# Kernel tuning notes

Measured on AMD Instinct MI355X. Metric: run time of the kernel, lower is better.

The kernel has to match this reference:

```python
import jax, jax.numpy as jnp
import numpy as np

B, T, DIM = 2, 2048, 2048
N_HEADS, N_KV_HEADS = 16, 4
HEAD_DIM = DIM // N_HEADS  # 128
N_REP = N_HEADS // N_KV_HEADS  # 4
ROPE_THETA = 10000.0


def setup_inputs() -> dict:
    key = jax.random.key(0)
    ks = jax.random.split(key, 5)
    x = jax.random.normal(ks[0], (B, T, DIM), dtype=jnp.float32)
    # RoPE tables (equivalent to complex freqs_cis = exp(i * t * inv_freq))
    inv_freq = 1.0 / (ROPE_THETA ** (np.arange(0, HEAD_DIM, 2, dtype=np.float32) / HEAD_DIM))
    t = np.arange(T, dtype=np.float32)
    ang = np.outer(t, inv_freq)  # (T, HEAD_DIM//2)
    freqs_cos = jnp.asarray(np.cos(ang), dtype=jnp.float32)
    freqs_sin = jnp.asarray(np.sin(ang), dtype=jnp.float32)
    s = 0.02
    wq = jax.random.normal(ks[1], (DIM, N_HEADS * HEAD_DIM), dtype=jnp.float32) * s
    wk = jax.random.normal(ks[2], (DIM, N_KV_HEADS * HEAD_DIM), dtype=jnp.float32) * s
    wv = jax.random.normal(ks[3], (DIM, N_KV_HEADS * HEAD_DIM), dtype=jnp.float32) * s
    wo = jax.random.normal(ks[4], (N_HEADS * HEAD_DIM, DIM), dtype=jnp.float32) * s
    return {"x": x, "freqs_cos": freqs_cos, "freqs_sin": freqs_sin,
            "wq": wq, "wk": wk, "wv": wv, "wo": wo}


def _apply_rope(t, cos, sin):
    # t: (B, H, T, hd); cos/sin: (T, hd//2); interleaved pairs like view_as_complex
    tr = t[..., 0::2]
    ti = t[..., 1::2]
    c = cos[None, None, :, :]
    s = sin[None, None, :, :]
    out_r = tr * c - ti * s
    out_i = tr * s + ti * c
    return jnp.stack([out_r, out_i], axis=-1).reshape(t.shape)


def reference(x, freqs_cos, freqs_sin, wq, wk, wv, wo):
    Bb, Tt, C = x.shape
    q = (x @ wq).reshape(Bb, Tt, N_HEADS, HEAD_DIM).transpose(0, 2, 1, 3)      # (B,H,T,hd)
    k = (x @ wk).reshape(Bb, Tt, N_KV_HEADS, HEAD_DIM).transpose(0, 2, 1, 3)   # (B,KV,T,hd)
    v = (x @ wv).reshape(Bb, Tt, N_KV_HEADS, HEAD_DIM).transpose(0, 2, 1, 3)
    q = _apply_rope(q, freqs_cos[:Tt], freqs_sin[:Tt])
    k = _apply_rope(k, freqs_cos[:Tt], freqs_sin[:Tt])
    # GQA repeat_kv
    k = jnp.repeat(k, N_REP, axis=1)  # (B,H,T,hd)
    v = jnp.repeat(v, N_REP, axis=1)
    scale = 1.0 / jnp.sqrt(jnp.float32(HEAD_DIM))
    scores = jnp.einsum("bhqd,bhkd->bhqk", q, k) * scale
    causal = jnp.tril(jnp.ones((Tt, Tt), dtype=bool))
    scores = jnp.where(causal[None, None], scores, jnp.float32(-jnp.inf))
    attn = jax.nn.softmax(scores, axis=-1)
    out = jnp.einsum("bhqk,bhkd->bhqd", attn, v)          # (B,H,T,hd)
    out = out.transpose(0, 2, 1, 3).reshape(Bb, Tt, C)
    return out @ wo
```

## Files before the change

### kernel.cpp

```cpp
#include <hip/hip_runtime.h>
#include <hip/hip_bf16.h>

#define SEQT 2048
#define NH 16
#define HD 128

typedef __bf16 bf16;
typedef __bf16 bf16x4 __attribute__((ext_vector_type(4)));
typedef __bf16 bf16x8 __attribute__((ext_vector_type(8)));
typedef float f32x4 __attribute__((ext_vector_type(4)));
typedef float f32x16 __attribute__((ext_vector_type(16)));

__device__ inline void glds16(const bf16* g, bf16* l) {
  __builtin_amdgcn_global_load_lds(
      (const __attribute__((address_space(1))) unsigned int*)g,
      (__attribute__((address_space(3))) unsigned int*)l, 16, 0, 0);
}

__device__ inline unsigned int cvtpk(float a, float b) {
  unsigned int d;
  asm("v_cvt_pk_bf16_f32 %0, %1, %2" : "=v"(d) : "v"(a), "v"(b));
  return d;
}

__global__ __launch_bounds__(256) void k_convert(const float* __restrict__ in,
                                                 bf16* __restrict__ out, int n8) {
  int i = blockIdx.x * 256 + threadIdx.x;
  if (i >= n8) return;
  const float4* p = (const float4*)in + (size_t)i * 2;
  float4 a = p[0], b = p[1];
  bf16x8 o;
  o[0] = (bf16)a.x; o[1] = (bf16)a.y; o[2] = (bf16)a.z; o[3] = (bf16)a.w;
  o[4] = (bf16)b.x; o[5] = (bf16)b.y; o[6] = (bf16)b.z; o[7] = (bf16)b.w;
  *((bf16x8*)out + i) = o;
}

__global__ __launch_bounds__(256) void k_transpose(const float* __restrict__ in,
                                                   bf16* __restrict__ out, int R, int C) {
  __shared__ float tile[32][33];
  int c0 = blockIdx.x * 32, r0 = blockIdx.y * 32;
  int tx = threadIdx.x, ty = threadIdx.y;
#pragma unroll
  for (int i = 0; i < 4; i++)
    tile[ty + i * 8][tx] = in[(size_t)(r0 + ty + i * 8) * C + c0 + tx];
  __syncthreads();
#pragma unroll
  for (int i = 0; i < 4; i++) {
    int r = ty + i * 8;
    out[(size_t)(c0 + r) * R + r0 + tx] = (bf16)tile[tx][r];
  }
}

__global__ __launch_bounds__(256) void k_transpose3(const float* __restrict__ wq,
                                                    const float* __restrict__ wk,
                                                    const float* __restrict__ wv,
                                                    bf16* __restrict__ W) {
  __shared__ float tile[32][33];
  int bx = blockIdx.x;
  const float* src;
  bf16* dst;
  int C;
  if (bx < 64) {
    src = wq; dst = W; C = 2048;
  } else if (bx < 80) {
    src = wk; dst = W + 2048 * 2048; C = 512; bx -= 64;
  } else {
    src = wv; dst = W + 2560 * 2048; C = 512; bx -= 80;
  }
  int c0 = bx * 32, r0 = blockIdx.y * 32;
  int tx = threadIdx.x, ty = threadIdx.y;
#pragma unroll
  for (int i = 0; i < 4; i++)
    tile[ty + i * 8][tx] = src[(size_t)(r0 + ty + i * 8) * C + c0 + tx];
  __syncthreads();
#pragma unroll
  for (int i = 0; i < 4; i++) {
    int r = ty + i * 8;
    dst[(size_t)(c0 + r) * 2048 + r0 + tx] = (bf16)tile[tx][r];
  }
}

template <typename OutT>
__global__ __launch_bounds__(512, 2) void k_gemm8(const bf16* __restrict__ A,
                                                  const bf16* __restrict__ Bt,
                                                  OutT* __restrict__ C,
                                                  int nbx, int K, int ldc) {
  __shared__ bf16 AB[2][2][16384];
  int nb = gridDim.x;
  int cpx = nb >> 3;
  int bid = blockIdx.x;
  int sw = (bid & 7) * cpx + (bid >> 3);
  int bx = sw % nbx, by = sw / nbx;
  int m0 = by << 8, n0 = bx << 8;
  int tid = threadIdx.x;
  int lane = tid & 63, wid = tid >> 6;
  int wr2 = wid >> 2, wc2 = wid & 3;
  int lr = lane & 15, lg = lane >> 4;
  int lx = lr & 7;

  f32x4 acc[2][4][2][2] = {};

  int srow = tid >> 3;
  int ssl8 = ((tid & 7) ^ (srow & 7)) * 8;

#define STAGE(SBUF, SAB, SHALF, KO)                                           \
  {                                                                           \
    int ko = (KO) <= (K - 64) ? (KO) : 0;                                     \
    const bf16* gb = (SAB) ? Bt : A;                                          \
    int rb = ((SAB) ? n0 : m0) + (SHALF) * 128 + srow;                        \
    glds16(gb + (size_t)rb * K + ko + ssl8,                                   \
           &AB[SBUF][SAB][(SHALF) * 8192 + tid * 8]);                         \
    glds16(gb + (size_t)(rb + 64) * K + ko + ssl8,                            \
           &AB[SBUF][SAB][(SHALF) * 8192 + (512 + tid) * 8]);                 \
  }

#define PHASE(BUF, QM, QN, SBUF, SAB, SHALF, SKO, DOVM)                       \
  {                                                                           \
    bf16x8 af[4][2], bq[2][2];                                                \
    _Pragma("unroll") for (int mi = 0; mi < 4; mi++)                          \
      _Pragma("unroll") for (int kk = 0; kk < 2; kk++)                        \
        af[mi][kk] = *(const bf16x8*)&AB[BUF][0][                             \
            ((QM) * 128 + wr2 * 64 + mi * 16 + lr) * 64 +                     \
            (((kk * 4 + lg) ^ lx) * 8)];                                      \
    _Pragma("unroll") for (int ni = 0; ni < 2; ni++)                          \
      _Pragma("unroll") for (int kk = 0; kk < 2; kk++)                        \
        bq[ni][kk] = *(const bf16x8*)&AB[BUF][1][                             \
            ((QN) * 128 + wc2 * 32 + ni * 16 + lr) * 64 +                     \
            (((kk * 4 + lg) ^ lx) * 8)];                                      \
    STAGE(SBUF, SAB, SHALF, SKO)                                              \
    if (DOVM) { asm volatile("s_waitcnt vmcnt(4)" ::: "memory"); }            \
    __builtin_amdgcn_sched_barrier(0);                                        \
    __builtin_amdgcn_s_barrier();                                             \
    __builtin_amdgcn_sched_barrier(0);                                        \
    __builtin_amdgcn_s_setprio(1);                                            \
    _Pragma("unroll") for (int kk = 0; kk < 2; kk++)                          \
      _Pragma("unroll") for (int mi = 0; mi < 4; mi++)                        \
        _Pragma("unroll") for (int ni = 0; ni < 2; ni++)                      \
          acc[QM][mi][QN][ni] = __builtin_amdgcn_mfma_f32_16x16x32_bf16(      \
              af[mi][kk], bq[ni][kk], acc[QM][mi][QN][ni], 0, 0, 0);          \
    __builtin_amdgcn_s_setprio(0);                                            \
    __builtin_amdgcn_sched_barrier(0);                                        \
    __builtin_amdgcn_s_barrier();                                             \
    __builtin_amdgcn_sched_barrier(0);                                        \
  }

  STAGE(0, 0, 0, 0) STAGE(0, 1, 0, 0) STAGE(0, 0, 1, 0) STAGE(0, 1, 1, 0)
  STAGE(1, 0, 0, 64) STAGE(1, 1, 0, 64)
  asm volatile("s_waitcnt vmcnt(4)" ::: "memory");
  __builtin_amdgcn_sched_barrier(0);
  __builtin_amdgcn_s_barrier();
  __builtin_amdgcn_sched_barrier(0);

  int nit = K >> 7;
  for (int it = 0; it < nit; it++) {
    int kb = it << 7;
    PHASE(0, 0, 0,  1, 0, 1, kb + 64,  0)
    PHASE(0, 0, 1,  1, 1, 1, kb + 64,  0)
    PHASE(0, 1, 0,  0, 0, 0, kb + 128, 0)
    PHASE(0, 1, 1,  0, 1, 0, kb + 128, 1)
    PHASE(1, 0, 0,  0, 0, 1, kb + 128, 0)
    PHASE(1, 0, 1,  0, 1, 1, kb + 128, 0)
    PHASE(1, 1, 0,  1, 0, 0, kb + 192, 0)
    PHASE(1, 1, 1,  1, 1, 0, kb + 192, 1)
  }
#undef PHASE
#undef STAGE

  int crow = m0 + wr2 * 64 + lg * 4;
  int ccol = n0 + wc2 * 32 + lr;
#pragma unroll
  for (int qm = 0; qm < 2; qm++)
#pragma unroll
    for (int mi = 0; mi < 4; mi++)
#pragma unroll
      for (int qn = 0; qn < 2; qn++)
#pragma unroll
        for (int ni = 0; ni < 2; ni++)
#pragma unroll
          for (int r = 0; r < 4; r++)
            C[(size_t)(crow + qm * 128 + mi * 16 + r) * ldc +
              ccol + qn * 128 + ni * 16] = (OutT)acc[qm][mi][qn][ni][r];
}

__global__ __launch_bounds__(256) void k_rope(bf16* __restrict__ qkv,
                                              const float* __restrict__ fcos,
                                              const float* __restrict__ fsin) {
  int gid = blockIdx.x * 256 + threadIdx.x;
  int row = gid / 1280;
  int p = gid % 1280;
  int head = p >> 6;
  int dp = p & 63;
  int t = row & (SEQT - 1);
  int colbase = head < NH ? head * HD : NH * HD + (head - NH) * HD;
  bf16* ptr = qkv + (size_t)row * 3072 + colbase + dp * 2;
  float a = (float)ptr[0], b = (float)ptr[1];
  float c = fcos[t * 64 + dp], s = fsin[t * 64 + dp];
  ptr[0] = (bf16)(a * c - b * s);
  ptr[1] = (bf16)(a * s + b * c);
}

__global__ __launch_bounds__(256, 2) void k_attn(const bf16* __restrict__ qkv,
                                                 bf16* __restrict__ attout) {
  __shared__ bf16 Kl[2][8192];
  __shared__ bf16 Vt[128][72];
  __shared__ float Tabs[4][4][32];
  int bid = blockIdx.x;
  int qt = 31 - (bid >> 5);
  int bh = bid & 31;
  int b = bh >> 4, h = bh & 15, kvh = h >> 2;
  int tid = threadIdx.x, wid = tid >> 6, lane = tid & 63;
  int kvhalf = wid >> 1, wq = wid & 1;
  int li = lane & 31, hi = lane >> 5;
  int q0 = qt * 64;
  int qmin = q0 + wq * 32, qmax = qmin + 31;
  int qlane = qmin + li;
  const float C1 = 0.12751744979927212f;

  const bf16* kgbase = qkv + (size_t)b * SEQT * 3072 + 2048 + kvh * HD;
  const bf16* vgbase = kgbase + 512;

  bf16x8 qf[8];
  {
    const bf16* qb = qkv + (size_t)(b * SEQT + qlane) * 3072 + h * HD + hi * 8;
#pragma unroll
    for (int ks = 0; ks < 8; ks++) qf[ks] = *(const bf16x8*)(qb + ks * 16);
  }

  float mrun = -INFINITY, lpart = 0.f;
  f32x16 o0 = {}, o1 = {}, o2 = {}, o3 = {};
  int nkt = qt + 1;
  int kvbase = 32 * kvhalf;

  int g = (lane >> 4) & 3;
  int lr = lane & 15;
  int kq4 = (wid * 4 + g) * 4;
  int dc = lr * 8;
  int xr = (lr & 7) << 3;
  int kvw = kq4 ^ xr;

  bf16x8 vr0, vr1, vr2, vr3;

#pragma unroll
  for (int r = 0; r < 4; r++) {
    int ci = r * 256 + tid;
    int row = ci >> 4;
    int sl = (ci & 15) ^ (row & 15);
    glds16(kgbase + (size_t)row * 3072 + sl * 8, &Kl[0][ci * 8]);
  }
  {
    const bf16* vrow = vgbase + (size_t)kq4 * 3072 + dc;
    vr0 = *(const bf16x8*)(vrow);
    vr1 = *(const bf16x8*)(vrow + 3072);
    vr2 = *(const bf16x8*)(vrow + 6144);
    vr3 = *(const bf16x8*)(vrow + 9216);
  }

  for (int kt = 0; kt < nkt; kt++) {
    int cur = kt & 1;
    int kv0 = kt * 64;
    asm volatile("s_waitcnt vmcnt(0)" ::: "memory");

#pragma unroll
    for (int j = 0; j < 8; j++) {
      bf16x4 w;
      w[0] = vr0[j]; w[1] = vr1[j]; w[2] = vr2[j]; w[3] = vr3[j];
      *(bf16x4*)&Vt[dc + j][kvw] = w;
    }

    if (kt + 1 < nkt) {
      int kv1 = kv0 + 64;
      bf16* kdst = &Kl[cur ^ 1][0];
#pragma unroll
      for (int r = 0; r < 4; r++) {
        int ci = r * 256 + tid;
        int row = ci >> 4;
        int sl = (ci & 15) ^ (row & 15);
        glds16(kgbase + (size_t)(kv1 + row) * 3072 + sl * 8, kdst + ci * 8);
      }
      const bf16* vrow = vgbase + (size_t)(kv1 + kq4) * 3072 + dc;
      vr0 = *(const bf16x8*)(vrow);
      vr1 = *(const bf16x8*)(vrow + 3072);
      vr2 = *(const bf16x8*)(vrow + 6144);
      vr3 = *(const bf16x8*)(vrow + 9216);
    }

    asm volatile("s_waitcnt lgkmcnt(0)" ::: "memory");
    __builtin_amdgcn_sched_barrier(0);
    __builtin_amdgcn_s_barrier();
    __builtin_amdgcn_sched_barrier(0);

    if (kv0 + kvbase <= qmax) {
      f32x16 s0 = {};
      const char* kb0 = (const char*)&Kl[cur][0] + kvhalf * 8192 + li * 256;
      __builtin_amdgcn_s_setprio(1);
#pragma unroll
      for (int ks = 0; ks < 8; ks++) {
        int off = ((ks * 2 + hi) ^ (li & 15)) << 4;
        bf16x8 kf0 = *(const bf16x8*)(kb0 + off);
        s0 = __builtin_amdgcn_mfma_f32_32x32x16_bf16(kf0, qf[ks], s0, 0, 0, 0);
      }
      __builtin_amdgcn_s_setprio(0);

      if (kv0 + kvbase + 31 > qmin) {
        int base0 = kv0 + kvbase + 4 * hi - qlane;
#pragma unroll
        for (int r = 0; r < 16; r++) {
          int off = (r & 3) + 8 * (r >> 2);
          if (base0 + off > 0) s0[r] = -INFINITY;
        }
      }

      float pm = s0[0];
#pragma unroll
      for (int r = 1; r < 16; r++) pm = fmaxf(pm, s0[r]);
      pm = fmaxf(pm, __shfl_xor(pm, 32));

      if (!__all(pm - mrun <= 62.0f)) {
        float mnew = fmaxf(mrun, pm);
        float alpha = exp2f((mrun - mnew) * C1);
        mrun = mnew;
        lpart *= alpha;
        Tabs[0][wid][li] = alpha;
        asm volatile("s_waitcnt lgkmcnt(0)" ::: "memory");
        f32x4 a0 = *(const f32x4*)&Tabs[0][wid][4 * hi];
        f32x4 a1 = *(const f32x4*)&Tabs[0][wid][4 * hi + 8];
        f32x4 a2 = *(const f32x4*)&Tabs[0][wid][4 * hi + 16];
        f32x4 a3 = *(const f32x4*)&Tabs[0][wid][4 * hi + 24];
#define RESC_RR(rr, av)                                            \
  _Pragma("unroll") for (int i = 0; i < 4; i++) {                  \
    float f = av[i];                                               \
    o0[rr * 4 + i] *= f; o1[rr * 4 + i] *= f;                      \
    o2[rr * 4 + i] *= f; o3[rr * 4 + i] *= f;                      \
  }
        RESC_RR(0, a0) RESC_RR(1, a1) RESC_RR(2, a2) RESC_RR(3, a3)
#undef RESC_RR
      }

      float mC = mrun * C1;
      float rs = 0.f;
#pragma unroll
      for (int r = 0; r < 16; r++) {
        float p = exp2f(fmaf(s0[r], C1, -mC));
        s0[r] = p; rs += p;
      }
      lpart += rs;

      union U4 { unsigned int u[4]; bf16x8 v; };
      U4 pa0, pa1;
      {
        unsigned int e0 = cvtpk(s0[0], s0[1]), e1 = cvtpk(s0[2], s0[3]);
        unsigned int e2 = cvtpk(s0[4], s0[5]), e3 = cvtpk(s0[6], s0[7]);
        unsigned int e4 = cvtpk(s0[8], s0[9]), e5 = cvtpk(s0[10], s0[11]);
        unsigned int e6 = cvtpk(s0[12], s0[13]), e7 = cvtpk(s0[14], s0[15]);
        unsigned int t0 = __shfl_xor(e0, 32), t1 = __shfl_xor(e1, 32);
        unsigned int t2 = __shfl_xor(e2, 32), t3 = __shfl_xor(e3, 32);
        unsigned int t4 = __shfl_xor(e4, 32), t5 = __shfl_xor(e5, 32);
        unsigned int t6 = __shfl_xor(e6, 32), t7 = __shfl_xor(e7, 32);
        pa0.u[0] = hi ? t2 : e0;  pa0.u[1] = hi ? t3 : e1;
        pa0.u[2] = hi ? e2 : t0;  pa0.u[3] = hi ? e3 : t1;
        pa1.u[0] = hi ? t6 : e4;  pa1.u[1] = hi ? t7 : e5;
        pa1.u[2] = hi ? e6 : t4;  pa1.u[3] = hi ? e7 : t5;
      }

      __builtin_amdgcn_s_setprio(1);
#define PV_DB(OACC, DB)                                                      \
  {                                                                          \
    int d = DB * 32 + li;                                                    \
    int xv = ((d >> 3) & 7) << 3;                                            \
    bf16x8 vb0 = *(const bf16x8*)&Vt[d][(kvbase + hi * 8) ^ xv];             \
    bf16x8 vb1 = *(const bf16x8*)&Vt[d][(kvbase + 16 + hi * 8) ^ xv];        \
    OACC = __builtin_amdgcn_mfma_f32_32x32x16_bf16(pa0.v, vb0, OACC, 0, 0, 0); \
    OACC = __builtin_amdgcn_mfma_f32_32x32x16_bf16(pa1.v, vb1, OACC, 0, 0, 0); \
  }
      PV_DB(o0, 0) PV_DB(o1, 1) PV_DB(o2, 2) PV_DB(o3, 3)
#undef PV_DB
      __builtin_amdgcn_s_setprio(0);
    }

    __builtin_amdgcn_sched_barrier(0);
    __builtin_amdgcn_s_barrier();
    __builtin_amdgcn_sched_barrier(0);
  }

  lpart += __shfl_xor(lpart, 32);
  Tabs[0][wid][li] = mrun;
  Tabs[1][wid][li] = lpart;
  asm volatile("s_waitcnt lgkmcnt(0)" ::: "memory");
  __builtin_amdgcn_s_barrier();
  int peer = wid ^ 2;
  float mP = Tabs[0][peer][li], lP = Tabs[1][peer][li];
  float mS = fmaxf(mrun, mP);
  float fMe = exp2f((mrun - mS) * C1);
  float fPe = exp2f((mP - mS) * C1);
  float lTot = lpart * fMe + lP * fPe;
  Tabs[2][wid][li] = fMe;
  Tabs[3][wid][li] = 1.f / lTot;
  asm volatile("s_waitcnt lgkmcnt(0)" ::: "memory");
  __builtin_amdgcn_s_barrier();
  f32x4 Fv0 = *(const f32x4*)&Tabs[2][wid][4 * hi];
  f32x4 Fv1 = *(const f32x4*)&Tabs[2][wid][4 * hi + 8];
  f32x4 Fv2 = *(const f32x4*)&Tabs[2][wid][4 * hi + 16];
  f32x4 Fv3 = *(const f32x4*)&Tabs[2][wid][4 * hi + 24];
  f32x4 Iv0 = *(const f32x4*)&Tabs[3][wid][4 * hi];
  f32x4 Iv1 = *(const f32x4*)&Tabs[3][wid][4 * hi + 8];
  f32x4 Iv2 = *(const f32x4*)&Tabs[3][wid][4 * hi + 16];
  f32x4 Iv3 = *(const f32x4*)&Tabs[3][wid][4 * hi + 24];

  float* X = (float*)&Kl[0][0];
  float* Xb = X + (wid & 1) * 4096;
  if (kvhalf == 1) {
#define XW_RR(OACC, DB, rr, Fv)                                              \
  _Pragma("unroll") for (int i = 0; i < 4; i++)                              \
    Xb[(4 * hi + 8 * rr + i) * 128 + DB * 32 + li] = OACC[rr * 4 + i] * Fv[i];
#define XW_DB(OACC, DB) XW_RR(OACC, DB, 0, Fv0) XW_RR(OACC, DB, 1, Fv1) \
                        XW_RR(OACC, DB, 2, Fv2) XW_RR(OACC, DB, 3, Fv3)
    XW_DB(o0, 0) XW_DB(o1, 1) XW_DB(o2, 2) XW_DB(o3, 3)
#undef XW_DB
#undef XW_RR
  }
  asm volatile("s_waitcnt lgkmcnt(0)" ::: "memory");
  __builtin_amdgcn_s_barrier();
  if (kvhalf == 0) {
#define XR_RR(OACC, DB, rr, Fv)                                              \
  _Pragma("unroll") for (int i = 0; i < 4; i++)                              \
    OACC[rr * 4 + i] = OACC[rr * 4 + i] * Fv[i] +                            \
        Xb[(4 * hi + 8 * rr + i) * 128 + DB * 32 + li];
#define XR_DB(OACC, DB) XR_RR(OACC, DB, 0, Fv0) XR_RR(OACC, DB, 1, Fv1) \
                        XR_RR(OACC, DB, 2, Fv2) XR_RR(OACC, DB, 3, Fv3)
    XR_DB(o0, 0) XR_DB(o1, 1) XR_DB(o2, 2) XR_DB(o3, 3)
#undef XR_DB
#undef XR_RR
    size_t obase = (size_t)(b * SEQT) * 2048 + h * HD;
#define STORE_RR(rr, lv)                                                     \
  _Pragma("unroll") for (int i = 0; i < 4; i++) {                            \
    int q = qmin + 4 * hi + 8 * rr + i;                                      \
    size_t rowb = obase + (size_t)q * 2048 + li;                             \
    attout[rowb + 0]  = (bf16)(o0[rr * 4 + i] * lv[i]);                      \
    attout[rowb + 32] = (bf16)(o1[rr * 4 + i] * lv[i]);                      \
    attout[rowb + 64] = (bf16)(o2[rr * 4 + i] * lv[i]);                      \
    attout[rowb + 96] = (bf16)(o3[rr * 4 + i] * lv[i]);                      \
  }
    STORE_RR(0, Iv0) STORE_RR(1, Iv1) STORE_RR(2, Iv2) STORE_RR(3, Iv3)
#undef STORE_RR
  }
}

extern "C" void kernel_launch(void* const* d_in, const int* in_sizes, int n_in,
                              void* d_out, int out_size, void* d_ws, size_t ws_size,
                              hipStream_t stream) {
  const float* x    = (const float*)d_in[0];
  const float* fcos = (const float*)d_in[1];
  const float* fsin = (const float*)d_in[2];
  const float* wq   = (const float*)d_in[3];
  const float* wk   = (const float*)d_in[4];
  const float* wv   = (const float*)d_in[5];
  const float* wo   = (const float*)d_in[6];
  float* out = (float*)d_out;

  char* ws = (char*)d_ws;
  bf16* XB  = (bf16*)ws;
  bf16* W   = (bf16*)(ws + 16777216);
  bf16* QKV = (bf16*)(ws + 16777216 + 12582912);

  dim3 tb(32, 8);
  k_transpose3<<<dim3(96, 64), tb, 0, stream>>>(wq, wk, wv, W);
  k_convert<<<4096, 256, 0, stream>>>(x, XB, 1048576);
  k_gemm8<bf16><<<192, 512, 0, stream>>>(XB, W, QKV, 12, 2048, 3072);
  k_rope<<<20480, 256, 0, stream>>>(QKV, fcos, fsin);
  k_attn<<<1024, 256, 0, stream>>>(QKV, XB);
  k_transpose<<<dim3(64, 64), tb, 0, stream>>>(wo, W, 2048, 2048);
  k_gemm8<float><<<128, 512, 0, stream>>>(XB, W, out, 8, 2048, 2048);
}
```

Baseline: 224.6 us.

## Double-buffer V tile to drop one barrier per step; vectorize RoPE kernel

The attention loop now keeps two transposed V tiles in shared memory, one per K buffer. This lets each iteration use a single barrier, placed after the V store and before the next prefetch, instead of two, so waves spend less time stalled at barriers. The RoPE kernel now has each thread process 16 bf16 elements with 16-byte vector loads and stores, and launches 8x fewer blocks. The cost is roughly 18 KB more LDS per block, which may reduce occupancy, plus a subtler cross-iteration hazard argument for buffer reuse.

Measured after the change: 225.1 us. Within noise of the previous version (+0.2%).

```diff
diff --git a/kernel.cpp b/kernel.cpp
--- a/kernel.cpp
+++ b/kernel.cpp
@@ -186,23 +186,36 @@
                                               const float* __restrict__ fcos,
                                               const float* __restrict__ fsin) {
   int gid = blockIdx.x * 256 + threadIdx.x;
-  int row = gid / 1280;
-  int p = gid % 1280;
-  int head = p >> 6;
-  int dp = p & 63;
+  int row = gid / 160;
+  int p = gid % 160;
+  int head = p >> 3;
+  int g8 = p & 7;
   int t = row & (SEQT - 1);
   int colbase = head < NH ? head * HD : NH * HD + (head - NH) * HD;
-  bf16* ptr = qkv + (size_t)row * 3072 + colbase + dp * 2;
-  float a = (float)ptr[0], b = (float)ptr[1];
-  float c = fcos[t * 64 + dp], s = fsin[t * 64 + dp];
-  ptr[0] = (bf16)(a * c - b * s);
-  ptr[1] = (bf16)(a * s + b * c);
+  bf16* ptr = qkv + (size_t)row * 3072 + colbase + g8 * 16;
+  bf16x8 v0 = *(const bf16x8*)ptr;
+  bf16x8 v1 = *(const bf16x8*)(ptr + 8);
+  const f32x4* cp = (const f32x4*)(fcos + t * 64 + g8 * 8);
+  const f32x4* sp = (const f32x4*)(fsin + t * 64 + g8 * 8);
+  f32x4 c0 = cp[0], c1 = cp[1], s0 = sp[0], s1 = sp[1];
+  bf16x8 o0, o1;
+#pragma unroll
+  for (int k = 0; k < 4; k++) {
+    float a0 = (float)v0[2 * k], b0 = (float)v0[2 * k + 1];
+    o0[2 * k]     = (bf16)(a0 * c0[k] - b0 * s0[k]);
+    o0[2 * k + 1] = (bf16)(a0 * s0[k] + b0 * c0[k]);
+    float a1 = (float)v1[2 * k], b1 = (float)v1[2 * k + 1];
+    o1[2 * k]     = (bf16)(a1 * c1[k] - b1 * s1[k]);
+    o1[2 * k + 1] = (bf16)(a1 * s1[k] + b1 * c1[k]);
+  }
+  *(bf16x8*)ptr = o0;
+  *(bf16x8*)(ptr + 8) = o1;
 }
 
 __global__ __launch_bounds__(256, 2) void k_attn(const bf16* __restrict__ qkv,
                                                  bf16* __restrict__ attout) {
   __shared__ bf16 Kl[2][8192];
-  __shared__ bf16 Vt[128][72];
+  __shared__ bf16 Vt[2][128][72];
   __shared__ float Tabs[4][4][32];
   int bid = blockIdx.x;
   int qt = 31 - (bid >> 5);
@@ -264,8 +277,13 @@
     for (int j = 0; j < 8; j++) {
       bf16x4 w;
       w[0] = vr0[j]; w[1] = vr1[j]; w[2] = vr2[j]; w[3] = vr3[j];
-      *(bf16x4*)&Vt[dc + j][kvw] = w;
+      *(bf16x4*)&Vt[cur][dc + j][kvw] = w;
     }
+
+    asm volatile("s_waitcnt lgkmcnt(0)" ::: "memory");
+    __builtin_amdgcn_sched_barrier(0);
+    __builtin_amdgcn_s_barrier();
+    __builtin_amdgcn_sched_barrier(0);
 
     if (kt + 1 < nkt) {
       int kv1 = kv0 + 64;
@@ -283,11 +301,6 @@
       vr2 = *(const bf16x8*)(vrow + 6144);
       vr3 = *(const bf16x8*)(vrow + 9216);
     }
-
-    asm volatile("s_waitcnt lgkmcnt(0)" ::: "memory");
-    __builtin_amdgcn_sched_barrier(0);
-    __builtin_amdgcn_s_barrier();
-    __builtin_amdgcn_sched_barrier(0);
 
     if (kv0 + kvbase <= qmax) {
       f32x16 s0 = {};
@@ -367,8 +380,8 @@
   {                                                                          \
     int d = DB * 32 + li;                                                    \
     int xv = ((d >> 3) & 7) << 3;                                            \
-    bf16x8 vb0 = *(const bf16x8*)&Vt[d][(kvbase + hi * 8) ^ xv];             \
-    bf16x8 vb1 = *(const bf16x8*)&Vt[d][(kvbase + 16 + hi * 8) ^ xv];        \
+    bf16x8 vb0 = *(const bf16x8*)&Vt[cur][d][(kvbase + hi * 8) ^ xv];        \
+    bf16x8 vb1 = *(const bf16x8*)&Vt[cur][d][(kvbase + 16 + hi * 8) ^ xv];   \
     OACC = __builtin_amdgcn_mfma_f32_32x32x16_bf16(pa0.v, vb0, OACC, 0, 0, 0); \
     OACC = __builtin_amdgcn_mfma_f32_32x32x16_bf16(pa1.v, vb1, OACC, 0, 0, 0); \
   }
@@ -376,10 +389,6 @@
 #undef PV_DB
       __builtin_amdgcn_s_setprio(0);
     }
-
-    __builtin_amdgcn_sched_barrier(0);
-    __builtin_amdgcn_s_barrier();
-    __builtin_amdgcn_sched_barrier(0);
   }
 
   lpart += __shfl_xor(lpart, 32);
@@ -466,7 +475,7 @@
   k_transpose3<<<dim3(96, 64), tb, 0, stream>>>(wq, wk, wv, W);
   k_convert<<<4096, 256, 0, stream>>>(x, XB, 1048576);
   k_gemm8<bf16><<<192, 512, 0, stream>>>(XB, W, QKV, 12, 2048, 3072);
-  k_rope<<<20480, 256, 0, stream>>>(QKV, fcos, fsin);
+  k_rope<<<2560, 256, 0, stream>>>(QKV, fcos, fsin);
   k_attn<<<1024, 256, 0, stream>>>(QKV, XB);
   k_transpose<<<dim3(64, 64), tb, 0, stream>>>(wo, W, 2048, 2048);
   k_gemm8<float><<<128, 512, 0, stream>>>(XB, W, out, 8, 2048, 2048);
```
